# Kernel optimization log

Measured on AMD Instinct MI355X. Metric: run time of the kernel, lower is better.

Reference implementation:

```python
import jax, jax.numpy as jnp
import numpy as np

EPS = 1e-5
SCALES = jnp.array([7.0, 7.0, 4.0], dtype=jnp.float32)  # (W, H, T) per source buffer
OUT_T, OUT_H, OUT_W = 3, 5, 5


def _roi_align3d(feat, start, end):
    """feat: [C,T,H,W]; start/end: [3] = (x, y, t). One sample per bin (bin center),
    trilinear interpolation, out-of-bounds -> 0 (standard ROIAlign convention)."""
    C, T, H, W = feat.shape
    dt = feat.dtype

    def centers(s, e, n):
        b = (e - s) / n
        return s + (jnp.arange(n, dtype=dt) + 0.5) * b

    xc = centers(start[0], end[0], OUT_W)  # [Wo]
    yc = centers(start[1], end[1], OUT_H)  # [Ho]
    tc = centers(start[2], end[2], OUT_T)  # [To]

    def prep(c, size):
        valid = ((c >= -1.0) & (c <= size)).astype(dt)
        c = jnp.clip(c, 0.0, size - 1)
        lo = jnp.floor(c).astype(jnp.int32)
        hi = jnp.minimum(lo + 1, size - 1)
        f = c - lo.astype(dt)
        return (lo, hi), ((1.0 - f) * valid, f * valid)

    ti, tw = prep(tc, T)
    yi, yw = prep(yc, H)
    xi, xw = prep(xc, W)

    out = jnp.zeros((C, OUT_T, OUT_H, OUT_W), dtype=dt)
    for a in range(2):
        for b in range(2):
            for c in range(2):
                g = feat[:, ti[a][:, None, None], yi[b][None, :, None], xi[c][None, None, :]]
                w = tw[a][:, None, None] * yw[b][None, :, None] * xw[c][None, None, :]
                out = out + g * w
    return out


def setup_inputs() -> dict:
    key = jax.random.key(0)
    k0, k1, k2 = jax.random.split(key, 3)
    B, C, T, H, W = 128, 1024, 4, 7, 7
    R = 256
    x = jax.random.normal(k0, (B, C, T, H, W), jnp.float32)
    w1 = jax.random.normal(k1, (R, C), jnp.float32) / np.sqrt(C).astype(np.float32)
    w2 = jax.random.normal(k2, (6, R), jnp.float32) / np.sqrt(R).astype(np.float32)
    return dict(
        x=x, w1=w1,
        g1=jnp.ones((R,), jnp.float32), b1=jnp.zeros((R,), jnp.float32),
        m1=jnp.zeros((R,), jnp.float32), v1=jnp.ones((R,), jnp.float32),
        w2=w2,
        g2=jnp.ones((6,), jnp.float32), b2=jnp.zeros((6,), jnp.float32),
        m2=jnp.zeros((6,), jnp.float32), v2=jnp.ones((6,), jnp.float32),
    )


def reference(x, w1, g1, b1, m1, v1, w2, g2, b2, m2, v2):
    # roi head: conv1x1x1 -> BN(eval) -> HSwish -> global avgpool -> conv1x1x1 -> BN(eval)
    h = jnp.einsum('bcthw,rc->brthw', x, w1)
    s1 = (g1 / jnp.sqrt(v1 + EPS))
    h = (h - m1[None, :, None, None, None]) * s1[None, :, None, None, None] + b1[None, :, None, None, None]
    h = h * jnp.clip(h + 3.0, 0.0, 6.0) * (1.0 / 6.0)  # HSwish
    h = h.mean(axis=(2, 3, 4))                          # AvgPool3d over full (T,H,W) -> [B,R]
    logits = h @ w2.T
    logits = (logits - m2) * (g2 / jnp.sqrt(v2 + EPS)) + b2  # [B,6]
    raw = jax.nn.sigmoid(logits)
    roi_start = 0.5 * raw[:, :3] * SCALES              # (x1,y1,t1)
    roi_end = (1.0 - 0.5 * raw[:, 3:]) * SCALES        # (x2,y2,t2)
    return jax.vmap(_roi_align3d)(x, roi_start, roi_end)  # [B,C,3,5,5]
```

## Files before the change

### kernel.cpp

```cpp
#include <hip/hip_runtime.h>

typedef __bf16 bf16x8 __attribute__((ext_vector_type(8)));
typedef __bf16 bf16x4 __attribute__((ext_vector_type(4)));
typedef float f32x4 __attribute__((ext_vector_type(4)));

#define EPS_F 1e-5f

__global__ __launch_bounds__(512) void k_gemm_pool(
    const float* __restrict__ x,
    const float* __restrict__ w1,
    const float* __restrict__ g1,
    const float* __restrict__ b1,
    const float* __restrict__ m1,
    const float* __restrict__ v1,
    float* __restrict__ pooled_part)
{
    constexpr int LDK = 40;
    __shared__ __bf16 Alds[2][112 * LDK];
    __shared__ float pool_lds[2][256];

    const int b   = blockIdx.x;
    const int mc  = blockIdx.y;
    const int tid = threadIdx.x;
    const int wave = tid >> 6, lane = tid & 63;
    const int wm = wave >> 2, wn = wave & 3;
    const int q  = lane >> 4, ln = lane & 15;
    const int nm = (wm == 0) ? 4 : 3;

    f32x4 acc[4][4];
#pragma unroll
    for (int i = 0; i < 4; i++)
#pragma unroll
        for (int j = 0; j < 4; j++) acc[i][j] = (f32x4){0.f, 0.f, 0.f, 0.f};

    const int c4  = tid & 7;
    const int p4  = tid >> 3;
    const bool a_act = (p4 < 28);
    const int  pg    = mc * 28 + p4;
    const bool a_val = a_act && (pg < 49);
    const float* xb = x + (size_t)b * (1024 * 196) + pg * 4;

    float fA[4][4];
    auto loadA = [&](int kc) {
        if (a_val) {
#pragma unroll
            for (int i = 0; i < 4; i++) {
                const float4 f = *(const float4*)(xb + (size_t)(kc + c4 * 4 + i) * 196);
                fA[i][0] = f.x; fA[i][1] = f.y; fA[i][2] = f.z; fA[i][3] = f.w;
            }
        } else {
#pragma unroll
            for (int i = 0; i < 4; i++)
#pragma unroll
                for (int j = 0; j < 4; j++) fA[i][j] = 0.f;
        }
    };
    auto storeA = [&](int buf) {
#pragma unroll
        for (int j = 0; j < 4; j++) {
            bf16x4 o = {(__bf16)fA[0][j], (__bf16)fA[1][j],
                        (__bf16)fA[2][j], (__bf16)fA[3][j]};
            *(bf16x4*)&Alds[buf][(p4 * 4 + j) * LDK + c4 * 4] = o;
        }
    };

    const float* wBr = w1 + (size_t)(wn * 64 + ln) * 1024 + q * 8;
    float4 fB[4][2];
    auto loadB = [&](int kc) {
#pragma unroll
        for (int ni = 0; ni < 4; ni++) {
            fB[ni][0] = *(const float4*)(wBr + ni * 16384 + kc);
            fB[ni][1] = *(const float4*)(wBr + ni * 16384 + kc + 4);
        }
    };

    if (a_act) { loadA(0); storeA(0); loadA(32); }
    loadB(0);
    asm volatile("s_waitcnt lgkmcnt(0)" ::: "memory");
    __builtin_amdgcn_s_barrier();

    for (int kc = 0, t = 0; kc < 1024; kc += 32, ++t) {
        const int cur = t & 1;
        bf16x8 bfr[4];
#pragma unroll
        for (int ni = 0; ni < 4; ni++)
            bfr[ni] = (bf16x8){(__bf16)fB[ni][0].x, (__bf16)fB[ni][0].y,
                               (__bf16)fB[ni][0].z, (__bf16)fB[ni][0].w,
                               (__bf16)fB[ni][1].x, (__bf16)fB[ni][1].y,
                               (__bf16)fB[ni][1].z, (__bf16)fB[ni][1].w};
        if (kc + 32 < 1024) loadB(kc + 32);
        if (a_act && kc + 32 < 1024) {
            storeA(cur ^ 1);
            if (kc + 64 < 1024) loadA(kc + 64);
        }
#pragma unroll
        for (int mi = 0; mi < 4; mi++) {
            if (mi < nm) {
                const bf16x8 af =
                    *(const bf16x8*)&Alds[cur][((wm * 4 + mi) * 16 + ln) * LDK + q * 8];
#pragma unroll
                for (int ni = 0; ni < 4; ni++)
                    acc[mi][ni] = __builtin_amdgcn_mfma_f32_16x16x32_bf16(
                        af, bfr[ni], acc[mi][ni], 0, 0, 0);
            }
        }
        asm volatile("s_waitcnt lgkmcnt(0)" ::: "memory");
        __builtin_amdgcn_s_barrier();
    }

    float psum[4] = {0.f, 0.f, 0.f, 0.f};
#pragma unroll
    for (int ni = 0; ni < 4; ni++) {
        const int r = (wn * 4 + ni) * 16 + ln;
        const float s1 = g1[r] * rsqrtf(v1[r] + EPS_F);
        const float mu = m1[r];
        const float be = b1[r];
#pragma unroll
        for (int mi = 0; mi < 4; mi++) {
            if (mi < nm) {
#pragma unroll
                for (int i = 0; i < 4; i++) {
                    const int m = mc * 112 + (wm * 4 + mi) * 16 + q * 4 + i;
                    if (m < 196) {
                        float v = acc[mi][ni][i];
                        v = (v - mu) * s1 + be;
                        const float g = fminf(fmaxf(v + 3.f, 0.f), 6.f);
                        psum[ni] += v * g * (1.f / 6.f);
                    }
                }
            }
        }
    }
#pragma unroll
    for (int ni = 0; ni < 4; ni++) {
        psum[ni] += __shfl_xor(psum[ni], 16, 64);
        psum[ni] += __shfl_xor(psum[ni], 32, 64);
    }
    if (lane < 16) {
#pragma unroll
        for (int ni = 0; ni < 4; ni++)
            pool_lds[wm][(wn * 4 + ni) * 16 + lane] = psum[ni];
    }
    __syncthreads();
    if (tid < 256)
        pooled_part[(size_t)mc * (128 * 256) + b * 256 + tid] =
            (pool_lds[0][tid] + pool_lds[1][tid]) * (1.f / 196.f);
}

__global__ __launch_bounds__(64) void k_logits(
    const float* __restrict__ pooled_part,
    const float* __restrict__ w2,
    const float* __restrict__ g2,
    const float* __restrict__ b2,
    const float* __restrict__ m2,
    const float* __restrict__ v2,
    float* __restrict__ roi)
{
    const int b = blockIdx.x, t = threadIdx.x;
    const float4 pa = ((const float4*)(pooled_part + b * 256))[t];
    const float4 pb = ((const float4*)(pooled_part + 128 * 256 + b * 256))[t];
    float4 p4;
    p4.x = pa.x + pb.x; p4.y = pa.y + pb.y;
    p4.z = pa.z + pb.z; p4.w = pa.w + pb.w;
    float part[6];
#pragma unroll
    for (int j = 0; j < 6; j++) {
        const float4 w = *(const float4*)(w2 + j * 256 + t * 4);
        part[j] = p4.x * w.x + p4.y * w.y + p4.z * w.z + p4.w * w.w;
    }
#pragma unroll
    for (int j = 0; j < 6; j++)
#pragma unroll
        for (int off = 32; off >= 1; off >>= 1)
            part[j] += __shfl_xor(part[j], off, 64);
    if (t == 0) {
        const float SC[3] = {7.f, 7.f, 4.f};
        float raw[6];
#pragma unroll
        for (int j = 0; j < 6; j++) {
            float l = part[j];
            const float s = g2[j] * rsqrtf(v2[j] + EPS_F);
            l = (l - m2[j]) * s + b2[j];
            raw[j] = 1.f / (1.f + expf(-l));
        }
#pragma unroll
        for (int d = 0; d < 3; d++) {
            roi[b * 6 + d]     = 0.5f * raw[d] * SC[d];
            roi[b * 6 + 3 + d] = (1.f - 0.5f * raw[3 + d]) * SC[d];
        }
    }
}

__device__ __forceinline__ void prep1(float s, float e, int n, int size, int i,
                                      int& lo, int& hi, float& w0, float& w1)
{
    const float bsz = (e - s) / (float)n;
    float c = s + ((float)i + 0.5f) * bsz;
    const float valid = (c >= -1.f && c <= (float)size) ? 1.f : 0.f;
    c = fminf(fmaxf(c, 0.f), (float)(size - 1));
    lo = (int)floorf(c);
    hi = min(lo + 1, size - 1);
    const float f = c - (float)lo;
    w0 = (1.f - f) * valid;
    w1 = f * valid;
}

__global__ __launch_bounds__(256) void k_roi(
    const float* __restrict__ x,
    const float* __restrict__ roi,
    float* __restrict__ out)
{
    __shared__ float xs[32 * 200];
    __shared__ int   soff[8][80];
    __shared__ float swt[8][80];

    const int b = blockIdx.x, c0 = blockIdx.y * 32;
    const int tid = threadIdx.x;

    const float* xb = x + ((size_t)b * 1024 + c0) * 196;
#pragma unroll
    for (int k = 0; k < 7; k++) {
        const int i4 = tid + k * 256;
        if (i4 < 1568) {
            const int c = i4 / 49, pq = i4 % 49;
            const float4 v = *(const float4*)(xb + c * 196 + pq * 4);
            *(float4*)&xs[c * 200 + pq * 4] = v;
        }
    }
    if (tid < 75) {
        const int po = tid;
        const int to = po / 25, rem = po % 25, yo = rem / 5, xo = rem % 5;
        const float sx = roi[b * 6 + 0], ex = roi[b * 6 + 3];
        const float sy = roi[b * 6 + 1], ey = roi[b * 6 + 4];
        const float st = roi[b * 6 + 2], et = roi[b * 6 + 5];
        int tl, th, yl, yh, xl, xh;
        float tw0, tw1, yw0, yw1, xw0, xw1;
        prep1(st, et, 3, 4, to, tl, th, tw0, tw1);
        prep1(sy, ey, 5, 7, yo, yl, yh, yw0, yw1);
        prep1(sx, ex, 5, 7, xo, xl, xh, xw0, xw1);
#pragma unroll
        for (int s = 0; s < 8; s++) {
            const int   ti = (s & 4) ? th : tl;
            const int   yi = (s & 2) ? yh : yl;
            const int   xi = (s & 1) ? xh : xl;
            const float w = ((s & 4) ? tw1 : tw0) *
                            ((s & 2) ? yw1 : yw0) *
                            ((s & 1) ? xw1 : xw0);
            soff[s][po] = ti * 49 + yi * 7 + xi;
            swt[s][po]  = w;
        }
    }
    __syncthreads();

    const size_t obase = ((size_t)b * 1024 + c0) * 75;
#pragma unroll
    for (int k = 0; k < 10; k++) {
        const int e = tid + k * 256;
        if (e < 2400) {
            const int c = e / 75, po = e % 75;
            const float* row = &xs[c * 200];
            float v = 0.f;
#pragma unroll
            for (int s = 0; s < 8; s++)
                v += swt[s][po] * row[soff[s][po]];
            out[obase + e] = v;
        }
    }
}

extern "C" void kernel_launch(void* const* d_in, const int* in_sizes, int n_in,
                              void* d_out, int out_size, void* d_ws, size_t ws_size,
                              hipStream_t stream)
{
    const float* x  = (const float*)d_in[0];
    const float* w1 = (const float*)d_in[1];
    const float* g1 = (const float*)d_in[2];
    const float* b1 = (const float*)d_in[3];
    const float* m1 = (const float*)d_in[4];
    const float* v1 = (const float*)d_in[5];
    const float* w2 = (const float*)d_in[6];
    const float* g2 = (const float*)d_in[7];
    const float* b2 = (const float*)d_in[8];
    const float* m2 = (const float*)d_in[9];
    const float* v2 = (const float*)d_in[10];

    float* pooled_part = (float*)d_ws;
    float* roi         = pooled_part + 2 * 128 * 256;
    float* out         = (float*)d_out;

    k_gemm_pool<<<dim3(128, 2), 512, 0, stream>>>(x, w1, g1, b1, m1, v1, pooled_part);
    k_logits<<<128, 64, 0, stream>>>(pooled_part, w2, g2, b2, m2, v2, roi);
    k_roi<<<dim3(128, 32), 256, 0, stream>>>(x, roi, out);
}
```

Baseline: 245.8 us.

## Prepack x and w1 to bf16 tiles and stream GEMM operands via global_load_lds

Adds pre-pass kernels that convert x and w1 to bf16 in k-tiled, MFMA-friendly layouts. The GEMM then loads both operands straight into double-buffered LDS with async global_load_lds and vmcnt waits. This removes per-thread fp32 loads, register conversion and LDS stores from the GEMM inner loop. In exchange, the whole of x is read an extra time and a bf16 copy is written to workspace.

```diff
diff --git a/kernel.cpp b/kernel.cpp
--- a/kernel.cpp
+++ b/kernel.cpp
@@ -1,22 +1,69 @@
 #include <hip/hip_runtime.h>
 
 typedef __bf16 bf16x8 __attribute__((ext_vector_type(8)));
-typedef __bf16 bf16x4 __attribute__((ext_vector_type(4)));
 typedef float f32x4 __attribute__((ext_vector_type(4)));
 
 #define EPS_F 1e-5f
 
+__device__ __forceinline__ void gload_lds16(const void* g, void* l) {
+    __builtin_amdgcn_global_load_lds(
+        (const __attribute__((address_space(1))) unsigned int*)g,
+        (__attribute__((address_space(3))) unsigned int*)l, 16, 0, 0);
+}
+
+__global__ __launch_bounds__(256) void k_pack_x(
+    const float* __restrict__ x, __bf16* __restrict__ xt)
+{
+    __shared__ float xs[32][204];
+    const int b = blockIdx.x, kt = blockIdx.y, tid = threadIdx.x;
+    const float* src = x + ((size_t)b * 1024 + (size_t)kt * 32) * 196;
+#pragma unroll
+    for (int k = 0; k < 7; k++) {
+        const int i4 = tid + k * 256;
+        if (i4 < 1568) {
+            const int c = i4 / 49, pq = i4 % 49;
+            const float4 v = *(const float4*)(src + c * 196 + pq * 4);
+            *(float4*)&xs[c][pq * 4] = v;
+        }
+    }
+    __syncthreads();
+    __bf16* dst = xt + (size_t)(b * 32 + kt) * 196 * 32;
+#pragma unroll
+    for (int k = 0; k < 4; k++) {
+        const int it = tid + k * 256;
+        if (it < 784) {
+            const int p = it >> 2, g = it & 3;
+            bf16x8 o;
+#pragma unroll
+            for (int j = 0; j < 8; j++) o[j] = (__bf16)xs[g * 8 + j][p];
+            *(bf16x8*)(dst + (size_t)p * 32 + g * 8) = o;
+        }
+    }
+}
+
+__global__ __launch_bounds__(256) void k_pack_w1(
+    const float* __restrict__ w1, __bf16* __restrict__ w1t)
+{
+    const int it = blockIdx.x * 256 + threadIdx.x;
+    const int kt = it >> 10, rem = it & 1023, r = rem >> 2, g = rem & 3;
+    const float* s = w1 + (size_t)r * 1024 + kt * 32 + g * 8;
+    bf16x8 o;
+#pragma unroll
+    for (int j = 0; j < 8; j++) o[j] = (__bf16)s[j];
+    *(bf16x8*)(w1t + (size_t)it * 8) = o;
+}
+
 __global__ __launch_bounds__(512) void k_gemm_pool(
-    const float* __restrict__ x,
-    const float* __restrict__ w1,
+    const __bf16* __restrict__ xt,
+    const __bf16* __restrict__ w1t,
     const float* __restrict__ g1,
     const float* __restrict__ b1,
     const float* __restrict__ m1,
     const float* __restrict__ v1,
     float* __restrict__ pooled_part)
 {
-    constexpr int LDK = 40;
-    __shared__ __bf16 Alds[2][112 * LDK];
+    __shared__ __bf16 Alds[2][4096];
+    __shared__ __bf16 Blds[2][8192];
     __shared__ float pool_lds[2][256];
 
     const int b   = blockIdx.x;
@@ -33,78 +80,43 @@
 #pragma unroll
         for (int j = 0; j < 4; j++) acc[i][j] = (f32x4){0.f, 0.f, 0.f, 0.f};
 
-    const int c4  = tid & 7;
-    const int p4  = tid >> 3;
-    const bool a_act = (p4 < 28);
-    const int  pg    = mc * 28 + p4;
-    const bool a_val = a_act && (pg < 49);
-    const float* xb = x + (size_t)b * (1024 * 196) + pg * 4;
-
-    float fA[4][4];
-    auto loadA = [&](int kc) {
-        if (a_val) {
-#pragma unroll
-            for (int i = 0; i < 4; i++) {
-                const float4 f = *(const float4*)(xb + (size_t)(kc + c4 * 4 + i) * 196);
-                fA[i][0] = f.x; fA[i][1] = f.y; fA[i][2] = f.z; fA[i][3] = f.w;
-            }
+    const __bf16* xa = xt + ((size_t)b * 32 * 196 + (size_t)mc * 112) * 32 + tid * 8;
+    const __bf16* wb = w1t + tid * 8;
+
+    auto issue = [&](int kt, int buf) {
+        gload_lds16(xa + (size_t)kt * (196 * 32), &Alds[buf][wave * 512]);
+        gload_lds16(wb + (size_t)kt * 8192,       &Blds[buf][wave * 512]);
+        gload_lds16(wb + (size_t)kt * 8192 + 4096, &Blds[buf][4096 + wave * 512]);
+    };
+
+    issue(0, 0);
+
+    for (int t = 0; t < 32; ++t) {
+        const int cur = t & 1;
+        if (t < 31) {
+            issue(t + 1, cur ^ 1);
+            asm volatile("s_waitcnt vmcnt(3)" ::: "memory");
         } else {
-#pragma unroll
-            for (int i = 0; i < 4; i++)
-#pragma unroll
-                for (int j = 0; j < 4; j++) fA[i][j] = 0.f;
-        }
-    };
-    auto storeA = [&](int buf) {
-#pragma unroll
-        for (int j = 0; j < 4; j++) {
-            bf16x4 o = {(__bf16)fA[0][j], (__bf16)fA[1][j],
-                        (__bf16)fA[2][j], (__bf16)fA[3][j]};
-            *(bf16x4*)&Alds[buf][(p4 * 4 + j) * LDK + c4 * 4] = o;
-        }
-    };
-
-    const float* wBr = w1 + (size_t)(wn * 64 + ln) * 1024 + q * 8;
-    float4 fB[4][2];
-    auto loadB = [&](int kc) {
-#pragma unroll
-        for (int ni = 0; ni < 4; ni++) {
-            fB[ni][0] = *(const float4*)(wBr + ni * 16384 + kc);
-            fB[ni][1] = *(const float4*)(wBr + ni * 16384 + kc + 4);
-        }
-    };
-
-    if (a_act) { loadA(0); storeA(0); loadA(32); }
-    loadB(0);
-    asm volatile("s_waitcnt lgkmcnt(0)" ::: "memory");
-    __builtin_amdgcn_s_barrier();
-
-    for (int kc = 0, t = 0; kc < 1024; kc += 32, ++t) {
-        const int cur = t & 1;
+            asm volatile("s_waitcnt vmcnt(0)" ::: "memory");
+        }
+        __builtin_amdgcn_s_barrier();
+        __builtin_amdgcn_sched_barrier(0);
         bf16x8 bfr[4];
 #pragma unroll
         for (int ni = 0; ni < 4; ni++)
-            bfr[ni] = (bf16x8){(__bf16)fB[ni][0].x, (__bf16)fB[ni][0].y,
-                               (__bf16)fB[ni][0].z, (__bf16)fB[ni][0].w,
-                               (__bf16)fB[ni][1].x, (__bf16)fB[ni][1].y,
-                               (__bf16)fB[ni][1].z, (__bf16)fB[ni][1].w};
-        if (kc + 32 < 1024) loadB(kc + 32);
-        if (a_act && kc + 32 < 1024) {
-            storeA(cur ^ 1);
-            if (kc + 64 < 1024) loadA(kc + 64);
-        }
+            bfr[ni] = *(const bf16x8*)&Blds[cur][(((wn * 4 + ni) * 16 + ln) * 32) + q * 8];
 #pragma unroll
         for (int mi = 0; mi < 4; mi++) {
             if (mi < nm) {
                 const bf16x8 af =
-                    *(const bf16x8*)&Alds[cur][((wm * 4 + mi) * 16 + ln) * LDK + q * 8];
+                    *(const bf16x8*)&Alds[cur][(((wm * 4 + mi) * 16 + ln) * 32) + q * 8];
 #pragma unroll
                 for (int ni = 0; ni < 4; ni++)
                     acc[mi][ni] = __builtin_amdgcn_mfma_f32_16x16x32_bf16(
                         af, bfr[ni], acc[mi][ni], 0, 0, 0);
             }
         }
-        asm volatile("s_waitcnt lgkmcnt(0)" ::: "memory");
+        __builtin_amdgcn_sched_barrier(0);
         __builtin_amdgcn_s_barrier();
     }
 
@@ -284,11 +296,16 @@
     const float* m2 = (const float*)d_in[9];
     const float* v2 = (const float*)d_in[10];
 
-    float* pooled_part = (float*)d_ws;
-    float* roi         = pooled_part + 2 * 128 * 256;
-    float* out         = (float*)d_out;
-
-    k_gemm_pool<<<dim3(128, 2), 512, 0, stream>>>(x, w1, g1, b1, m1, v1, pooled_part);
-    k_logits<<<128, 64, 0, stream>>>(pooled_part, w2, g2, b2, m2, v2, roi);
+    char* wsb = (char*)d_ws;
+    __bf16* xt     = (__bf16*)wsb;
+    __bf16* w1t    = (__bf16*)(wsb + 51388416);
+    float*  pooled = (float*)(wsb + 51912704);
+    float*  roi    = (float*)(wsb + 52174848);
+    float*  out    = (float*)d_out;
+
+    k_pack_w1<<<128, 256, 0, stream>>>(w1, w1t);
+    k_pack_x<<<dim3(128, 32), 256, 0, stream>>>(x, xt);
+    k_gemm_pool<<<dim3(128, 2), 512, 0, stream>>>(xt, w1t, g1, b1, m1, v1, pooled);
+    k_logits<<<128, 64, 0, stream>>>(pooled, w2, g2, b2, m2, v2, roi);
     k_roi<<<dim3(128, 32), 256, 0, stream>>>(x, roi, out);
 }
```

Measured after the change: 248.8 us. Within noise of the previous version (+1.2%).

## Split GEMM over output halves, fuse logits into ROI kernel, reorder A stores

Applied to the files above, without the earlier changes.

The GEMM-pool kernel now runs 512 blocks instead of 256, each computing half of the 256 output channels, and uses launch bounds that allow four blocks per CU. This is meant to fill more of the GPU's CUs and raise occupancy, though each block now reloads the full A tile for only half the work. The separate logits kernel is removed. Each ROI block recomputes the six ROI coordinates from the pooled partial sums, which removes one kernel launch and one dependency at the cost of redundant per-block work. LDS stores for A are also moved after the MFMAs, with sched barriers added to control instruction ordering.

```diff
diff --git a/kernel.cpp b/kernel.cpp
--- a/kernel.cpp
+++ b/kernel.cpp
@@ -6,7 +6,7 @@
 
 #define EPS_F 1e-5f
 
-__global__ __launch_bounds__(512) void k_gemm_pool(
+__global__ __launch_bounds__(512, 4) void k_gemm_pool(
     const float* __restrict__ x,
     const float* __restrict__ w1,
     const float* __restrict__ g1,
@@ -17,21 +17,23 @@
 {
     constexpr int LDK = 40;
     __shared__ __bf16 Alds[2][112 * LDK];
-    __shared__ float pool_lds[2][256];
-
-    const int b   = blockIdx.x;
-    const int mc  = blockIdx.y;
+    __shared__ float pool_lds[2][128];
+
+    const int bid = blockIdx.x;
+    const int b   = bid & 127;
+    const int mc  = (bid >> 7) & 1;
+    const int nh  = bid >> 8;
     const int tid = threadIdx.x;
     const int wave = tid >> 6, lane = tid & 63;
     const int wm = wave >> 2, wn = wave & 3;
     const int q  = lane >> 4, ln = lane & 15;
     const int nm = (wm == 0) ? 4 : 3;
 
-    f32x4 acc[4][4];
+    f32x4 acc[4][2];
 #pragma unroll
     for (int i = 0; i < 4; i++)
 #pragma unroll
-        for (int j = 0; j < 4; j++) acc[i][j] = (f32x4){0.f, 0.f, 0.f, 0.f};
+        for (int j = 0; j < 2; j++) acc[i][j] = (f32x4){0.f, 0.f, 0.f, 0.f};
 
     const int c4  = tid & 7;
     const int p4  = tid >> 3;
@@ -56,62 +58,68 @@
         }
     };
     auto storeA = [&](int buf) {
-#pragma unroll
-        for (int j = 0; j < 4; j++) {
-            bf16x4 o = {(__bf16)fA[0][j], (__bf16)fA[1][j],
-                        (__bf16)fA[2][j], (__bf16)fA[3][j]};
-            *(bf16x4*)&Alds[buf][(p4 * 4 + j) * LDK + c4 * 4] = o;
+        if (a_act) {
+#pragma unroll
+            for (int j = 0; j < 4; j++) {
+                bf16x4 o = {(__bf16)fA[0][j], (__bf16)fA[1][j],
+                            (__bf16)fA[2][j], (__bf16)fA[3][j]};
+                *(bf16x4*)&Alds[buf][(p4 * 4 + j) * LDK + c4 * 4] = o;
+            }
         }
     };
 
-    const float* wBr = w1 + (size_t)(wn * 64 + ln) * 1024 + q * 8;
-    float4 fB[4][2];
+    const float* wBr = w1 + (size_t)(nh * 128 + wn * 32 + ln) * 1024 + q * 8;
+    float4 fB[2][2];
     auto loadB = [&](int kc) {
 #pragma unroll
-        for (int ni = 0; ni < 4; ni++) {
+        for (int ni = 0; ni < 2; ni++) {
             fB[ni][0] = *(const float4*)(wBr + ni * 16384 + kc);
             fB[ni][1] = *(const float4*)(wBr + ni * 16384 + kc + 4);
         }
     };
 
-    if (a_act) { loadA(0); storeA(0); loadA(32); }
+    loadA(0);
+    storeA(0);
+    loadA(32);
     loadB(0);
     asm volatile("s_waitcnt lgkmcnt(0)" ::: "memory");
     __builtin_amdgcn_s_barrier();
 
-    for (int kc = 0, t = 0; kc < 1024; kc += 32, ++t) {
-        const int cur = t & 1;
-        bf16x8 bfr[4];
-#pragma unroll
-        for (int ni = 0; ni < 4; ni++)
+    for (int t = 0; t < 32; ++t) {
+        const int kc = t * 32;
+        bf16x8 bfr[2];
+#pragma unroll
+        for (int ni = 0; ni < 2; ni++)
             bfr[ni] = (bf16x8){(__bf16)fB[ni][0].x, (__bf16)fB[ni][0].y,
                                (__bf16)fB[ni][0].z, (__bf16)fB[ni][0].w,
                                (__bf16)fB[ni][1].x, (__bf16)fB[ni][1].y,
                                (__bf16)fB[ni][1].z, (__bf16)fB[ni][1].w};
-        if (kc + 32 < 1024) loadB(kc + 32);
-        if (a_act && kc + 32 < 1024) {
-            storeA(cur ^ 1);
-            if (kc + 64 < 1024) loadA(kc + 64);
-        }
+        if (t < 31) loadB(kc + 32);
 #pragma unroll
         for (int mi = 0; mi < 4; mi++) {
             if (mi < nm) {
                 const bf16x8 af =
-                    *(const bf16x8*)&Alds[cur][((wm * 4 + mi) * 16 + ln) * LDK + q * 8];
-#pragma unroll
-                for (int ni = 0; ni < 4; ni++)
+                    *(const bf16x8*)&Alds[t & 1][((wm * 4 + mi) * 16 + ln) * LDK + q * 8];
+#pragma unroll
+                for (int ni = 0; ni < 2; ni++)
                     acc[mi][ni] = __builtin_amdgcn_mfma_f32_16x16x32_bf16(
                         af, bfr[ni], acc[mi][ni], 0, 0, 0);
             }
         }
+        if (t < 31) {
+            storeA((t + 1) & 1);
+            if (t < 30) loadA(kc + 64);
+        }
         asm volatile("s_waitcnt lgkmcnt(0)" ::: "memory");
+        __builtin_amdgcn_sched_barrier(0);
         __builtin_amdgcn_s_barrier();
-    }
-
-    float psum[4] = {0.f, 0.f, 0.f, 0.f};
-#pragma unroll
-    for (int ni = 0; ni < 4; ni++) {
-        const int r = (wn * 4 + ni) * 16 + ln;
+        __builtin_amdgcn_sched_barrier(0);
+    }
+
+    float psum[2] = {0.f, 0.f};
+#pragma unroll
+    for (int ni = 0; ni < 2; ni++) {
+        const int r = nh * 128 + (wn * 2 + ni) * 16 + ln;
         const float s1 = g1[r] * rsqrtf(v1[r] + EPS_F);
         const float mu = m1[r];
         const float be = b1[r];
@@ -132,63 +140,19 @@
         }
     }
 #pragma unroll
-    for (int ni = 0; ni < 4; ni++) {
+    for (int ni = 0; ni < 2; ni++) {
         psum[ni] += __shfl_xor(psum[ni], 16, 64);
         psum[ni] += __shfl_xor(psum[ni], 32, 64);
     }
     if (lane < 16) {
 #pragma unroll
-        for (int ni = 0; ni < 4; ni++)
-            pool_lds[wm][(wn * 4 + ni) * 16 + lane] = psum[ni];
+        for (int ni = 0; ni < 2; ni++)
+            pool_lds[wm][(wn * 2 + ni) * 16 + lane] = psum[ni];
     }
     __syncthreads();
-    if (tid < 256)
-        pooled_part[(size_t)mc * (128 * 256) + b * 256 + tid] =
+    if (tid < 128)
+        pooled_part[(size_t)mc * (128 * 256) + b * 256 + nh * 128 + tid] =
             (pool_lds[0][tid] + pool_lds[1][tid]) * (1.f / 196.f);
-}
-
-__global__ __launch_bounds__(64) void k_logits(
-    const float* __restrict__ pooled_part,
-    const float* __restrict__ w2,
-    const float* __restrict__ g2,
-    const float* __restrict__ b2,
-    const float* __restrict__ m2,
-    const float* __restrict__ v2,
-    float* __restrict__ roi)
-{
-    const int b = blockIdx.x, t = threadIdx.x;
-    const float4 pa = ((const float4*)(pooled_part + b * 256))[t];
-    const float4 pb = ((const float4*)(pooled_part + 128 * 256 + b * 256))[t];
-    float4 p4;
-    p4.x = pa.x + pb.x; p4.y = pa.y + pb.y;
-    p4.z = pa.z + pb.z; p4.w = pa.w + pb.w;
-    float part[6];
-#pragma unroll
-    for (int j = 0; j < 6; j++) {
-        const float4 w = *(const float4*)(w2 + j * 256 + t * 4);
-        part[j] = p4.x * w.x + p4.y * w.y + p4.z * w.z + p4.w * w.w;
-    }
-#pragma unroll
-    for (int j = 0; j < 6; j++)
-#pragma unroll
-        for (int off = 32; off >= 1; off >>= 1)
-            part[j] += __shfl_xor(part[j], off, 64);
-    if (t == 0) {
-        const float SC[3] = {7.f, 7.f, 4.f};
-        float raw[6];
-#pragma unroll
-        for (int j = 0; j < 6; j++) {
-            float l = part[j];
-            const float s = g2[j] * rsqrtf(v2[j] + EPS_F);
-            l = (l - m2[j]) * s + b2[j];
-            raw[j] = 1.f / (1.f + expf(-l));
-        }
-#pragma unroll
-        for (int d = 0; d < 3; d++) {
-            roi[b * 6 + d]     = 0.5f * raw[d] * SC[d];
-            roi[b * 6 + 3 + d] = (1.f - 0.5f * raw[3 + d]) * SC[d];
-        }
-    }
 }
 
 __device__ __forceinline__ void prep1(float s, float e, int n, int size, int i,
@@ -207,12 +171,18 @@
 
 __global__ __launch_bounds__(256) void k_roi(
     const float* __restrict__ x,
-    const float* __restrict__ roi,
+    const float* __restrict__ pooled_part,
+    const float* __restrict__ w2,
+    const float* __restrict__ g2,
+    const float* __restrict__ b2,
+    const float* __restrict__ m2,
+    const float* __restrict__ v2,
     float* __restrict__ out)
 {
     __shared__ float xs[32 * 200];
     __shared__ int   soff[8][80];
     __shared__ float swt[8][80];
+    __shared__ float roi_s[6];
 
     const int b = blockIdx.x, c0 = blockIdx.y * 32;
     const int tid = threadIdx.x;
@@ -227,17 +197,45 @@
             *(float4*)&xs[c * 200 + pq * 4] = v;
         }
     }
+    if (tid < 64) {
+        const float4 pa = ((const float4*)(pooled_part + b * 256))[tid];
+        const float4 pb = ((const float4*)(pooled_part + 128 * 256 + b * 256))[tid];
+        float4 p4;
+        p4.x = pa.x + pb.x; p4.y = pa.y + pb.y;
+        p4.z = pa.z + pb.z; p4.w = pa.w + pb.w;
+        float part[6];
+#pragma unroll
+        for (int j = 0; j < 6; j++) {
+            const float4 w = *(const float4*)(w2 + j * 256 + tid * 4);
+            part[j] = p4.x * w.x + p4.y * w.y + p4.z * w.z + p4.w * w.w;
+        }
+#pragma unroll
+        for (int j = 0; j < 6; j++)
+#pragma unroll
+            for (int off = 32; off >= 1; off >>= 1)
+                part[j] += __shfl_xor(part[j], off, 64);
+        if (tid == 0) {
+            const float SC[3] = {7.f, 7.f, 4.f};
+#pragma unroll
+            for (int j = 0; j < 6; j++) {
+                float l = part[j];
+                const float s = g2[j] * rsqrtf(v2[j] + EPS_F);
+                l = (l - m2[j]) * s + b2[j];
+                const float raw = 1.f / (1.f + expf(-l));
+                roi_s[j] = (j < 3) ? 0.5f * raw * SC[j]
+                                   : (1.f - 0.5f * raw) * SC[j - 3];
+            }
+        }
+    }
+    __syncthreads();
     if (tid < 75) {
         const int po = tid;
         const int to = po / 25, rem = po % 25, yo = rem / 5, xo = rem % 5;
-        const float sx = roi[b * 6 + 0], ex = roi[b * 6 + 3];
-        const float sy = roi[b * 6 + 1], ey = roi[b * 6 + 4];
-        const float st = roi[b * 6 + 2], et = roi[b * 6 + 5];
         int tl, th, yl, yh, xl, xh;
         float tw0, tw1, yw0, yw1, xw0, xw1;
-        prep1(st, et, 3, 4, to, tl, th, tw0, tw1);
-        prep1(sy, ey, 5, 7, yo, yl, yh, yw0, yw1);
-        prep1(sx, ex, 5, 7, xo, xl, xh, xw0, xw1);
+        prep1(roi_s[2], roi_s[5], 3, 4, to, tl, th, tw0, tw1);
+        prep1(roi_s[1], roi_s[4], 5, 7, yo, yl, yh, yw0, yw1);
+        prep1(roi_s[0], roi_s[3], 5, 7, xo, xl, xh, xw0, xw1);
 #pragma unroll
         for (int s = 0; s < 8; s++) {
             const int   ti = (s & 4) ? th : tl;
@@ -284,11 +282,9 @@
     const float* m2 = (const float*)d_in[9];
     const float* v2 = (const float*)d_in[10];
 
-    float* pooled_part = (float*)d_ws;
-    float* roi         = pooled_part + 2 * 128 * 256;
-    float* out         = (float*)d_out;
-
-    k_gemm_pool<<<dim3(128, 2), 512, 0, stream>>>(x, w1, g1, b1, m1, v1, pooled_part);
-    k_logits<<<128, 64, 0, stream>>>(pooled_part, w2, g2, b2, m2, v2, roi);
-    k_roi<<<dim3(128, 32), 256, 0, stream>>>(x, roi, out);
-}
+    float* pooled = (float*)d_ws;
+    float* out    = (float*)d_out;
+
+    k_gemm_pool<<<512, 512, 0, stream>>>(x, w1, g1, b1, m1, v1, pooled);
+    k_roi<<<dim3(128, 32), 256, 0, stream>>>(x, pooled, w2, g2, b2, m2, v2, out);
+}
```

Result: slower. 258.7 us (+5.2%).
